# Performance work log

Measured on AMD Instinct MI355X. Metric: run time of the kernel, lower is better.

The kernel has to match this reference:

```python
import jax, jax.numpy as jnp
import numpy as np

N_EMBD = 1024
N_HEAD = 16
HEAD_SIZE = 64


def setup_inputs() -> dict:
    key = jax.random.key(0)
    ks = jax.random.split(key, 6)
    B, T, C, H, D = 2, 2048, N_EMBD, N_HEAD, HEAD_SIZE
    s = 1.0 / np.sqrt(C)
    x = jax.random.normal(ks[0], (B, T, C), dtype=jnp.float32)
    Wq = jax.random.normal(ks[1], (H, C, D), dtype=jnp.float32) * s
    Wk = jax.random.normal(ks[2], (H, C, D), dtype=jnp.float32) * s
    Wv = jax.random.normal(ks[3], (H, C, D), dtype=jnp.float32) * s
    Wo = jax.random.normal(ks[4], (H * D, C), dtype=jnp.float32) * (1.0 / np.sqrt(H * D))
    bo = jax.random.normal(ks[5], (C,), dtype=jnp.float32) * 0.01
    return {"x": x, "Wq": Wq, "Wk": Wk, "Wv": Wv, "Wo": Wo, "bo": bo}


def reference(x, Wq, Wk, Wv, Wo, bo):
    B, T, C = x.shape
    H, _, D = Wq.shape
    # Per-head projections, batched across heads: [B,H,T,D]
    q = jnp.einsum('btc,hcd->bhtd', x, Wq)
    k = jnp.einsum('btc,hcd->bhtd', x, Wk)
    v = jnp.einsum('btc,hcd->bhtd', x, Wv)
    # NOTE: original scales by sqrt(C) = sqrt(n_embd), not sqrt(head_size)
    scale = 1.0 / jnp.sqrt(jnp.float32(C))
    att = jnp.einsum('bhtd,bhsd->bhts', q, k) * scale  # [B,H,T,T]
    causal = jnp.tril(jnp.ones((T, T), dtype=bool))
    att = jnp.where(causal, att, -jnp.inf)
    att = jax.nn.softmax(att, axis=-1)
    # dropout omitted (eval mode / deterministic reference)
    out = jnp.einsum('bhts,bhsd->bhtd', att, v)  # [B,H,T,D]
    out = out.transpose(0, 2, 1, 3).reshape(B, T, H * D)
    return out @ Wo + bo
```

## Files before the change

### kernel.cpp

```cpp
#include <hip/hip_runtime.h>
#include <hip/hip_bf16.h>


typedef __hip_bfloat16 bf16;
typedef __bf16 v8bf __attribute__((ext_vector_type(8)));
typedef float  v4f  __attribute__((ext_vector_type(4)));
typedef unsigned long long u64;
typedef unsigned int u32;

#define MFMA16(a, b, c) __builtin_amdgcn_mfma_f32_16x16x32_bf16((a), (b), (c), 0, 0, 0)

__device__ __forceinline__ bf16 f2b(float x) { return __float2bfloat16(x); }
__device__ __forceinline__ __bf16 f2braw(float x) {
  bf16 t = __float2bfloat16(x);
  return *reinterpret_cast<__bf16*>(&t);
}
__device__ __forceinline__ unsigned short f2bu(float x) {
  bf16 t = __float2bfloat16(x);
  return *reinterpret_cast<unsigned short*>(&t);
}

__device__ __forceinline__ void load16_lds(const bf16* gptr, const bf16* lptr) {
  __builtin_amdgcn_global_load_lds(
      (const __attribute__((address_space(1))) u32*)gptr,
      (__attribute__((address_space(3))) u32*)lptr, 16, 0, 0);
}

__global__ __launch_bounds__(256) void prep_kernel(
    const float* __restrict__ x,
    const float* __restrict__ Wq, const float* __restrict__ Wk,
    const float* __restrict__ Wv, const float* __restrict__ Wo,
    bf16* __restrict__ xb, bf16* __restrict__ wt, bf16* __restrict__ wot)
{
  __shared__ float Lt[32][33];
  const int bid = blockIdx.x, tid = threadIdx.x;

  if (bid < 2048) {
    size_t i = ((size_t)bid * 256 + tid) * 8;
    float4 f0 = *(const float4*)(x + i);
    float4 f1 = *(const float4*)(x + i + 4);
    v8bf v;
    v[0] = f2braw(f0.x); v[1] = f2braw(f0.y); v[2] = f2braw(f0.z); v[3] = f2braw(f0.w);
    v[4] = f2braw(f1.x); v[5] = f2braw(f1.y); v[6] = f2braw(f1.z); v[7] = f2braw(f1.w);
    *(v8bf*)(xb + i) = v;
    return;
  }
  const int tx = tid & 31, ty = tid >> 5;
  if (bid < 5120) {
    const int idx = bid - 2048;
    const int z = idx >> 6, rem = idx & 63;
    const int p = z >> 4, h = z & 15;
    const float* ib = ((p == 0) ? Wq : (p == 1) ? Wk : Wv) + (size_t)h * 65536;
    bf16* ob = wt + (size_t)z * 65536;
    const int j0 = (rem & 1) * 32, i0 = (rem >> 1) * 32;
    #pragma unroll
    for (int r = 0; r < 4; ++r)
      Lt[ty + 8 * r][tx] = ib[(size_t)(i0 + ty + 8 * r) * 64 + j0 + tx];
    __syncthreads();
    #pragma unroll
    for (int r = 0; r < 4; ++r)
      ob[(size_t)(j0 + ty + 8 * r) * 1024 + i0 + tx] = f2b(Lt[tx][ty + 8 * r]);
  } else {
    const int idx = bid - 5120;
    const int j0 = (idx & 31) * 32, i0 = (idx >> 5) * 32;
    #pragma unroll
    for (int r = 0; r < 4; ++r)
      Lt[ty + 8 * r][tx] = Wo[(size_t)(i0 + ty + 8 * r) * 1024 + j0 + tx];
    __syncthreads();
    #pragma unroll
    for (int r = 0; r < 4; ++r)
      wot[(size_t)(j0 + ty + 8 * r) * 1024 + i0 + tx] = f2b(Lt[tx][ty + 8 * r]);
  }
}

__global__ __launch_bounds__(512, 2) void qkv_gemm_kernel(
    const bf16* __restrict__ xb, const bf16* __restrict__ wt,
    bf16* __restrict__ qkv)
{
  __shared__ __align__(16) bf16 Ash[3][256][32];
  __shared__ __align__(16) bf16 Bsh[3][256][32];

  const int mt = blockIdx.x, nt = blockIdx.y;
  const int tid = threadIdx.x, wid = tid >> 6, lane = tid & 63;
  const int ln = lane & 15, quad = lane >> 4;
  const int wm = wid >> 1, wn = wid & 1;
  const int m0 = mt * 256, n0 = nt * 192;

  const v4f vzero = {0.f, 0.f, 0.f, 0.f};
  v4f acc[4][6];
  #pragma unroll
  for (int mf = 0; mf < 4; ++mf)
    #pragma unroll
    for (int nf = 0; nf < 6; ++nf) acc[mf][nf] = vzero;

  const int srow = lane >> 2;
  const int sseg = ((lane & 3) ^ ((lane >> 3) & 3)) * 8;
  const int arow = wid * 32 + srow;
  const int br0 = wid * 32 + srow,  brow0 = (br0 < 192) ? br0 : 191;
  const int br1 = wid * 32 + 16 + srow, brow1 = (br1 < 192) ? br1 : 191;
  const bf16* ga  = xb + (size_t)(m0 + arow) * 1024 + sseg;
  const bf16* gb0 = wt + (size_t)(n0 + brow0) * 1024 + sseg;
  const bf16* gb1 = wt + (size_t)(n0 + brow1) * 1024 + sseg;

  const int fseg = (quad ^ ((ln >> 1) & 3)) * 8;

  #define QSTAGE(BUF) {                                          \
    load16_lds(ga,              &Ash[BUF][wid * 32][0]);         \
    load16_lds(ga + 16 * 1024,  &Ash[BUF][wid * 32 + 16][0]);    \
    load16_lds(gb0,             &Bsh[BUF][wid * 32][0]);         \
    load16_lds(gb1,             &Bsh[BUF][wid * 32 + 16][0]);    \
    ga += 32; gb0 += 32; gb1 += 32; }

  QSTAGE(0)
  QSTAGE(1)

  #define QSTEP(BUF, VM, DOSTAGE)                                          \
  {                                                                        \
    asm volatile("s_waitcnt vmcnt(" #VM ") lgkmcnt(0)" ::: "memory");      \
    __builtin_amdgcn_s_barrier();                                          \
    __builtin_amdgcn_sched_barrier(0);                                     \
    v8bf af[4], bfv[6];                                                    \
    _Pragma("unroll")                                                      \
    for (int mf = 0; mf < 4; ++mf)                                         \
      af[mf] = *(const v8bf*)&Ash[BUF][wm * 64 + mf * 16 + ln][fseg];      \
    _Pragma("unroll")                                                      \
    for (int nf = 0; nf < 6; ++nf)                                         \
      bfv[nf] = *(const v8bf*)&Bsh[BUF][wn * 96 + nf * 16 + ln][fseg];     \
    if (DOSTAGE) QSTAGE((BUF + 2) % 3)                                     \
    __builtin_amdgcn_s_setprio(1);                                         \
    _Pragma("unroll")                                                      \
    for (int mf = 0; mf < 4; ++mf)                                         \
      _Pragma("unroll")                                                    \
      for (int nf = 0; nf < 6; ++nf)                                       \
        acc[mf][nf] = MFMA16(af[mf], bfv[nf], acc[mf][nf]);                \
    __builtin_amdgcn_s_setprio(0);                                         \
  }

  #pragma unroll 1
  for (int it = 0; it < 10; ++it) {
    QSTEP(0, 4, 1)
    QSTEP(1, 4, 1)
    QSTEP(2, 4, 1)
  }
  QSTEP(0, 4, 0)
  QSTEP(1, 0, 0)
  #undef QSTEP
  #undef QSTAGE

  #pragma unroll
  for (int nf = 0; nf < 6; ++nf) {
    const int j = n0 + wn * 96 + nf * 16 + ln;
    const int p = j >> 10;
    const int h = (j >> 6) & 15;
    const int d = j & 63;
    if (p < 2) {
      const float scale = (p == 0) ? 0.0450841149f : 1.0f;
      bf16* base = qkv + (size_t)p * 4194304 + (size_t)h * 262144;
      #pragma unroll
      for (int mf = 0; mf < 4; ++mf)
        #pragma unroll
        for (int r = 0; r < 4; ++r) {
          int m = m0 + wm * 64 + mf * 16 + quad * 4 + r;
          base[(size_t)m * 64 + d] = f2b(acc[mf][nf][r] * scale);
        }
    } else {
      bf16* vb = qkv + (size_t)2 * 4194304 + (size_t)h * 262144;
      #pragma unroll
      for (int mf = 0; mf < 4; ++mf) {
        int mrow = m0 + wm * 64 + mf * 16 + quad * 4;
        int bi = mrow >> 11, t0 = mrow & 2047;
        u64 pk = (u64)f2bu(acc[mf][nf][0]) |
                 ((u64)f2bu(acc[mf][nf][1]) << 16) |
                 ((u64)f2bu(acc[mf][nf][2]) << 32) |
                 ((u64)f2bu(acc[mf][nf][3]) << 48);
        *(u64*)(vb + (size_t)bi * 131072 + (size_t)d * 2048 + t0) = pk;
      }
    }
  }
}

__global__ __launch_bounds__(256, 4) void attn_kernel(
    const bf16* __restrict__ qkv, bf16* __restrict__ att)
{
  union ShU {
    struct { bf16 K[2][64][64]; bf16 V[2][64][64]; } t;
    struct { float O[2][64][36]; float L[2][36]; } c;
  };
  __shared__ __align__(16) ShU sh;

  const int fid = blockIdx.x;
  const int j = fid >> 5;
  const int jr = j & 7, jq = j >> 3;
  const int mt = (jq == 0) ? (31 - jr) : (jq == 1) ? (8 + jr)
               : (jq == 2) ? (23 - jr) : jr;
  const int grp = fid & 31;
  const int b = grp >> 4, h = grp & 15;

  const int tid = threadIdx.x, w = tid >> 6, lane = tid & 63;
  const int ln = lane & 15, quad = lane >> 4;
  const int qh = w & 1, kh = w >> 1;

  const bf16* qbase  = qkv + (size_t)h * 262144 + (size_t)b * 131072;
  const bf16* kbase  = qbase + 4194304;
  const bf16* vtbase = qbase + 8388608;

  const int l8 = lane & 7, r8 = lane >> 3;
  const int slot = l8 ^ r8;
  const int p0 = w * 16 + r8, p1 = p0 + 8;
  const int kp0 = (p0 & 32) | ((p0 & 12) << 1) | ((p0 & 16) >> 2) | (p0 & 3);
  const int kp1 = (p1 & 32) | ((p1 & 12) << 1) | ((p1 & 16) >> 2) | (p1 & 3);
  const bf16* gkp0 = kbase + kp0 * 64 + slot * 8;
  const bf16* gkp1 = kbase + kp1 * 64 + slot * 8;
  const bf16* gvp0 = vtbase + p0 * 2048 + slot * 8;
  const bf16* gvp1 = gvp0 + 8 * 2048;

  const int sw = ln & 7;
  const int cc0 = ((quad    ) ^ sw) * 8;
  const int cc1 = ((quad + 4) ^ sw) * 8;
  const int cck = kh ? cc1 : cc0;
  const int krow0 = (kh * 32 + ln) * 64;
  const int ka0 = krow0 + cc0, ka1 = krow0 + cc1;
  const int voff = ln * 64 + cck;

  v8bf vone;
  {
    unsigned short u = 0x3F80;
    __bf16 e = *reinterpret_cast<__bf16*>(&u);
    #pragma unroll
    for (int jj = 0; jj < 8; ++jj) vone[jj] = e;
  }
  const v4f vzero = {0.f, 0.f, 0.f, 0.f};
  const float NEG = -30000.0f;

  #define STAGE2(BUF) {                                          \
    load16_lds(gkp0, &sh.t.K[BUF][w * 16][0]);                   \
    load16_lds(gkp1, &sh.t.K[BUF][w * 16 + 8][0]);               \
    load16_lds(gvp0, &sh.t.V[BUF][w * 16][0]);                   \
    load16_lds(gvp1, &sh.t.V[BUF][w * 16 + 8][0]);               \
    gkp0 += 4096; gkp1 += 4096; gvp0 += 64; gvp1 += 64; }

  const int row0 = mt * 64;
  const int qrow = row0 + qh * 32;

  v8bf aq[2][2];
  #pragma unroll
  for (int mc = 0; mc < 2; ++mc)
    #pragma unroll
    for (int ks = 0; ks < 2; ++ks)
      aq[mc][ks] = *(const v8bf*)(qbase +
          (size_t)(qrow + mc * 16 + ln) * 64 + ks * 32 + quad * 8);

  v4f o[2][4], lacc[2];
  #pragma unroll
  for (int mc = 0; mc < 2; ++mc) {
    lacc[mc] = vzero;
    #pragma unroll
    for (int dt = 0; dt < 4; ++dt) o[mc][dt] = vzero;
  }

  const int kb_end = mt;
  int kb = 0;
  STAGE2(0)

  #define TILE(BUF)                                                        \
  {                                                                        \
    __syncthreads();                                    \
    const bf16* krB = &sh.t.K[BUF][0][0];                                  \
    const bf16* vrB = &sh.t.V[BUF][0][0];                                  \
    v8bf kf[2][2], vf[4];                                                  \
    kf[0][0] = *(const v8bf*)(krB + ka0);                                  \
    kf[1][0] = *(const v8bf*)(krB + ka1);                                  \
    kf[0][1] = *(const v8bf*)(krB + ka0 + 1024);                           \
    kf[1][1] = *(const v8bf*)(krB + ka1 + 1024);                           \
    vf[0] = *(const v8bf*)(vrB + voff);                                    \
    vf[1] = *(const v8bf*)(vrB + voff + 1024);                             \
    vf[2] = *(const v8bf*)(vrB + voff + 2048);                             \
    vf[3] = *(const v8bf*)(vrB + voff + 3072);                             \
    if (kb < kb_end) STAGE2(BUF ^ 1)                                       \
    _Pragma("unroll")                                                      \
    for (int mc = 0; mc < 2; ++mc) {                                       \
      __builtin_amdgcn_s_setprio(1);                                       \
      v4f s[2];                                                            \
      s[0] = vzero; s[1] = vzero;                                          \
      _Pragma("unroll")                                                    \
      for (int ks = 0; ks < 2; ++ks) {                                     \
        s[0] = MFMA16(kf[ks][0], aq[mc][ks], s[0]);                        \
        s[1] = MFMA16(kf[ks][1], aq[mc][ks], s[1]);                        \
      }                                                                    \
      __builtin_amdgcn_s_setprio(0);                                       \
      const int qg = qrow + mc * 16 + ln;                                  \
      if (kb == kb_end) {                      \
        _Pragma("unroll")                                                  \
        for (int nfl = 0; nfl < 2; ++nfl) {                                \
          const int kc = kb * 64 + kh * 32 + quad * 8 + nfl * 4;           \
          _Pragma("unroll")                                                \
          for (int r = 0; r < 4; ++r)                                      \
            if (kc + r > qg) s[nfl][r] = NEG;                              \
        }                                                                  \
      }                                                                    \
      float ex[2][4];                                                      \
      _Pragma("unroll")                                                    \
      for (int nfl = 0; nfl < 2; ++nfl)                                    \
        _Pragma("unroll")                                                  \
        for (int r = 0; r < 4; ++r)                                        \
          ex[nfl][r] = exp2f(s[nfl][r]);                                   \
      union { u32 uw[4]; v8bf v; } pu;                                     \
      _Pragma("unroll")                                                    \
      for (int nfl = 0; nfl < 2; ++nfl)                                    \
        _Pragma("unroll")                                                  \
        for (int wi = 0; wi < 2; ++wi)                                     \
          asm("v_cvt_pk_bf16_f32 %0, %1, %2"                               \
              : "=v"(pu.uw[nfl * 2 + wi])                                  \
              : "v"(ex[nfl][2 * wi]), "v"(ex[nfl][2 * wi + 1]));           \
      __builtin_amdgcn_s_setprio(1);                                       \
      lacc[mc] = MFMA16(pu.v, vone, lacc[mc]);                             \
      _Pragma("unroll")                                                    \
      for (int dt = 0; dt < 4; ++dt)                                       \
        o[mc][dt] = MFMA16(pu.v, vf[dt], o[mc][dt]);                       \
      __builtin_amdgcn_s_setprio(0);                                       \
    }                                                                      \
  }

  while (true) {
    TILE(0)
    if (kb >= kb_end) break;
    ++kb;
    TILE(1)
    if (kb >= kb_end) break;
    ++kb;
  }
  #undef TILE
  #undef STAGE2

  __syncthreads();
  if (kh == 1) {
    #pragma unroll
    for (int mc = 0; mc < 2; ++mc) {
      #pragma unroll
      for (int dt = 0; dt < 4; ++dt)
        *(v4f*)&sh.c.O[qh][dt * 16 + ln][mc * 16 + quad * 4] = o[mc][dt];
      if (ln == 0)
        *(v4f*)&sh.c.L[qh][mc * 16 + quad * 4] = lacc[mc];
    }
  }
  __syncthreads();
  if (kh == 0) {
    #pragma unroll
    for (int mc = 0; mc < 2; ++mc) {
      v4f pl = *(const v4f*)&sh.c.L[qh][mc * 16 + quad * 4];
      v4f inv;
      #pragma unroll
      for (int r = 0; r < 4; ++r) inv[r] = 1.0f / (lacc[mc][r] + pl[r]);
      #pragma unroll
      for (int dt = 0; dt < 4; ++dt) {
        v4f po = *(const v4f*)&sh.c.O[qh][dt * 16 + ln][mc * 16 + quad * 4];
        #pragma unroll
        for (int r = 0; r < 4; ++r) {
          int m = b * 2048 + qrow + mc * 16 + quad * 4 + r;
          att[(size_t)m * 1024 + h * 64 + dt * 16 + ln] =
              f2b((o[mc][dt][r] + po[r]) * inv[r]);
        }
      }
    }
  }
}

__global__ __launch_bounds__(256) void out_gemm_kernel(
    const bf16* __restrict__ att, const bf16* __restrict__ wot,
    const float* __restrict__ bo, float* __restrict__ out)
{
  __shared__ __align__(16) bf16 Ash[2][128][32];
  __shared__ __align__(16) bf16 Bsh[2][64][32];

  const int mt = blockIdx.x, nt = blockIdx.y;
  const int tid = threadIdx.x, w = tid >> 6, lane = tid & 63;
  const int ln = lane & 15, quad = lane >> 4;
  const int wm = w >> 1, wn = w & 1;
  const int m0 = mt * 128, n0 = nt * 64;

  const v4f vzero = {0.f, 0.f, 0.f, 0.f};
  v4f acc[4][2];
  #pragma unroll
  for (int mf = 0; mf < 4; ++mf)
    #pragma unroll
    for (int nf = 0; nf < 2; ++nf) acc[mf][nf] = vzero;

  const int srow = lane >> 2;
  const int sseg = ((lane & 3) ^ ((lane >> 3) & 3)) * 8;
  const bf16* ga = att + (size_t)(m0 + 32 * w + srow) * 1024 + sseg;
  const bf16* gb = wot + (size_t)(n0 + 16 * w + srow) * 1024 + sseg;

  const int fseg = (quad ^ ((ln >> 1) & 3)) * 8;

  load16_lds(ga,             &Ash[0][32 * w][0]);
  load16_lds(ga + 16 * 1024, &Ash[0][32 * w + 16][0]);
  load16_lds(gb,             &Bsh[0][16 * w][0]);
  ga += 32; gb += 32;

  int kt = 0;
  #define OTILE(BUF)                                                     \
  {                                                                      \
    __syncthreads();                                                     \
    v8bf af[4], bfv[2];                                                  \
    _Pragma("unroll")                                                    \
    for (int mf = 0; mf < 4; ++mf)                                       \
      af[mf] = *(const v8bf*)&Ash[BUF][wm * 64 + mf * 16 + ln][fseg];    \
    _Pragma("unroll")                                                    \
    for (int nf = 0; nf < 2; ++nf)                                       \
      bfv[nf] = *(const v8bf*)&Bsh[BUF][wn * 32 + nf * 16 + ln][fseg];   \
    if (kt < 31) {                                                       \
      load16_lds(ga,             &Ash[BUF ^ 1][32 * w][0]);              \
      load16_lds(ga + 16 * 1024, &Ash[BUF ^ 1][32 * w + 16][0]);         \
      load16_lds(gb,             &Bsh[BUF ^ 1][16 * w][0]);              \
      ga += 32; gb += 32;                                                \
    }                                                                    \
    _Pragma("unroll")                                                    \
    for (int mf = 0; mf < 4; ++mf)                                       \
      _Pragma("unroll")                                                  \
      for (int nf = 0; nf < 2; ++nf)                                     \
        acc[mf][nf] = MFMA16(af[mf], bfv[nf], acc[mf][nf]);              \
    ++kt;                                                                \
  }

  #pragma unroll 1
  for (int it = 0; it < 16; ++it) {
    OTILE(0)
    OTILE(1)
  }
  #undef OTILE

  #pragma unroll
  for (int nf = 0; nf < 2; ++nf) {
    int j = n0 + wn * 32 + nf * 16 + ln;
    float bias = bo[j];
    #pragma unroll
    for (int mf = 0; mf < 4; ++mf)
      #pragma unroll
      for (int r = 0; r < 4; ++r) {
        int m = m0 + wm * 64 + mf * 16 + quad * 4 + r;
        out[(size_t)m * 1024 + j] = acc[mf][nf][r] + bias;
      }
  }
}

extern "C" void kernel_launch(void* const* d_in, const int* in_sizes, int n_in,
                              void* d_out, int out_size, void* d_ws, size_t ws_size,
                              hipStream_t stream) {
  const float* x  = (const float*)d_in[0];
  const float* Wq = (const float*)d_in[1];
  const float* Wk = (const float*)d_in[2];
  const float* Wv = (const float*)d_in[3];
  const float* Wo = (const float*)d_in[4];
  const float* bo = (const float*)d_in[5];
  float* out = (float*)d_out;

  bf16* xb  = (bf16*)d_ws;
  bf16* wt  = xb + 4194304;
  bf16* wot = xb + 7340032;
  bf16* qkv = xb + 8388608;
  bf16* att = xb + 20971520;

  prep_kernel<<<6144, 256, 0, stream>>>(x, Wq, Wk, Wv, Wo, xb, wt, wot);
  qkv_gemm_kernel<<<dim3(16, 16), 512, 0, stream>>>(xb, wt, qkv);
  attn_kernel<<<1024, 256, 0, stream>>>(qkv, att);
  out_gemm_kernel<<<dim3(32, 16), 256, 0, stream>>>(att, wot, bo, out);
}
```

Measured before the change: 165.5 us.

## Load V fragments directly from global and triple-buffer output GEMM pipeline

The attention kernel stops staging V tiles through LDS and instead loads each lane's V fragments straight from global memory (transposed V layout), halving the LDS footprint and the async copies per tile. The output projection GEMM moves from double to triple buffering with explicit vmcnt waits and raw barriers, so two stages of loads stay in flight, and it raises wave priority around the MFMA block. The risk is that direct global V loads are exposed to memory latency inside the tile loop without LDS prefetch. The hand-written waitcnt counts must also match the issued loads exactly.

```diff
diff --git a/kernel.cpp b/kernel.cpp
--- a/kernel.cpp
+++ b/kernel.cpp
@@ -183,7 +183,7 @@
     const bf16* __restrict__ qkv, bf16* __restrict__ att)
 {
   union ShU {
-    struct { bf16 K[2][64][64]; bf16 V[2][64][64]; } t;
+    struct { bf16 K[2][64][64]; } t;
     struct { float O[2][64][36]; float L[2][36]; } c;
   };
   __shared__ __align__(16) ShU sh;
@@ -211,16 +211,13 @@
   const int kp1 = (p1 & 32) | ((p1 & 12) << 1) | ((p1 & 16) >> 2) | (p1 & 3);
   const bf16* gkp0 = kbase + kp0 * 64 + slot * 8;
   const bf16* gkp1 = kbase + kp1 * 64 + slot * 8;
-  const bf16* gvp0 = vtbase + p0 * 2048 + slot * 8;
-  const bf16* gvp1 = gvp0 + 8 * 2048;
 
   const int sw = ln & 7;
   const int cc0 = ((quad    ) ^ sw) * 8;
   const int cc1 = ((quad + 4) ^ sw) * 8;
-  const int cck = kh ? cc1 : cc0;
   const int krow0 = (kh * 32 + ln) * 64;
   const int ka0 = krow0 + cc0, ka1 = krow0 + cc1;
-  const int voff = ln * 64 + cck;
+  const bf16* gvf = vtbase + (size_t)ln * 2048 + kh * 32 + quad * 8;
 
   v8bf vone;
   {
@@ -235,9 +232,7 @@
   #define STAGE2(BUF) {                                          \
     load16_lds(gkp0, &sh.t.K[BUF][w * 16][0]);                   \
     load16_lds(gkp1, &sh.t.K[BUF][w * 16 + 8][0]);               \
-    load16_lds(gvp0, &sh.t.V[BUF][w * 16][0]);                   \
-    load16_lds(gvp1, &sh.t.V[BUF][w * 16 + 8][0]);               \
-    gkp0 += 4096; gkp1 += 4096; gvp0 += 64; gvp1 += 64; }
+    gkp0 += 4096; gkp1 += 4096; }
 
   const int row0 = mt * 64;
   const int qrow = row0 + qh * 32;
@@ -266,16 +261,16 @@
   {                                                                        \
     __syncthreads();                                    \
     const bf16* krB = &sh.t.K[BUF][0][0];                                  \
-    const bf16* vrB = &sh.t.V[BUF][0][0];                                  \
     v8bf kf[2][2], vf[4];                                                  \
     kf[0][0] = *(const v8bf*)(krB + ka0);                                  \
     kf[1][0] = *(const v8bf*)(krB + ka1);                                  \
     kf[0][1] = *(const v8bf*)(krB + ka0 + 1024);                           \
     kf[1][1] = *(const v8bf*)(krB + ka1 + 1024);                           \
-    vf[0] = *(const v8bf*)(vrB + voff);                                    \
-    vf[1] = *(const v8bf*)(vrB + voff + 1024);                             \
-    vf[2] = *(const v8bf*)(vrB + voff + 2048);                             \
-    vf[3] = *(const v8bf*)(vrB + voff + 3072);                             \
+    vf[0] = *(const v8bf*)(gvf);                                           \
+    vf[1] = *(const v8bf*)(gvf + 32768);                                   \
+    vf[2] = *(const v8bf*)(gvf + 65536);                                   \
+    vf[3] = *(const v8bf*)(gvf + 98304);                                   \
+    gvf += 64;                                                             \
     if (kb < kb_end) STAGE2(BUF ^ 1)                                       \
     _Pragma("unroll")                                                      \
     for (int mc = 0; mc < 2; ++mc) {                                       \
@@ -369,8 +364,8 @@
     const bf16* __restrict__ att, const bf16* __restrict__ wot,
     const float* __restrict__ bo, float* __restrict__ out)
 {
-  __shared__ __align__(16) bf16 Ash[2][128][32];
-  __shared__ __align__(16) bf16 Bsh[2][64][32];
+  __shared__ __align__(16) bf16 Ash[3][128][32];
+  __shared__ __align__(16) bf16 Bsh[3][64][32];
 
   const int mt = blockIdx.x, nt = blockIdx.y;
   const int tid = threadIdx.x, w = tid >> 6, lane = tid & 63;
@@ -392,42 +387,47 @@
 
   const int fseg = (quad ^ ((ln >> 1) & 3)) * 8;
 
-  load16_lds(ga,             &Ash[0][32 * w][0]);
-  load16_lds(ga + 16 * 1024, &Ash[0][32 * w + 16][0]);
-  load16_lds(gb,             &Bsh[0][16 * w][0]);
-  ga += 32; gb += 32;
-
-  int kt = 0;
-  #define OTILE(BUF)                                                     \
-  {                                                                      \
-    __syncthreads();                                                     \
-    v8bf af[4], bfv[2];                                                  \
-    _Pragma("unroll")                                                    \
-    for (int mf = 0; mf < 4; ++mf)                                       \
-      af[mf] = *(const v8bf*)&Ash[BUF][wm * 64 + mf * 16 + ln][fseg];    \
-    _Pragma("unroll")                                                    \
-    for (int nf = 0; nf < 2; ++nf)                                       \
-      bfv[nf] = *(const v8bf*)&Bsh[BUF][wn * 32 + nf * 16 + ln][fseg];   \
-    if (kt < 31) {                                                       \
-      load16_lds(ga,             &Ash[BUF ^ 1][32 * w][0]);              \
-      load16_lds(ga + 16 * 1024, &Ash[BUF ^ 1][32 * w + 16][0]);         \
-      load16_lds(gb,             &Bsh[BUF ^ 1][16 * w][0]);              \
-      ga += 32; gb += 32;                                                \
-    }                                                                    \
-    _Pragma("unroll")                                                    \
-    for (int mf = 0; mf < 4; ++mf)                                       \
-      _Pragma("unroll")                                                  \
-      for (int nf = 0; nf < 2; ++nf)                                     \
-        acc[mf][nf] = MFMA16(af[mf], bfv[nf], acc[mf][nf]);              \
-    ++kt;                                                                \
+  #define OSTAGE(BUF) {                                          \
+    load16_lds(ga,             &Ash[BUF][32 * w][0]);            \
+    load16_lds(ga + 16 * 1024, &Ash[BUF][32 * w + 16][0]);       \
+    load16_lds(gb,             &Bsh[BUF][16 * w][0]);            \
+    ga += 32; gb += 32; }
+
+  OSTAGE(0)
+  OSTAGE(1)
+
+  #define OSTEP(BUF, VM, DOSTAGE)                                          \
+  {                                                                        \
+    asm volatile("s_waitcnt vmcnt(" #VM ") lgkmcnt(0)" ::: "memory");      \
+    __builtin_amdgcn_s_barrier();                                          \
+    __builtin_amdgcn_sched_barrier(0);                                     \
+    v8bf af[4], bfv[2];                                                    \
+    _Pragma("unroll")                                                      \
+    for (int mf = 0; mf < 4; ++mf)                                         \
+      af[mf] = *(const v8bf*)&Ash[BUF][wm * 64 + mf * 16 + ln][fseg];      \
+    _Pragma("unroll")                                                      \
+    for (int nf = 0; nf < 2; ++nf)                                         \
+      bfv[nf] = *(const v8bf*)&Bsh[BUF][wn * 32 + nf * 16 + ln][fseg];     \
+    if (DOSTAGE) OSTAGE((BUF + 2) % 3)                                     \
+    __builtin_amdgcn_s_setprio(1);                                         \
+    _Pragma("unroll")                                                      \
+    for (int mf = 0; mf < 4; ++mf)                                         \
+      _Pragma("unroll")                                                    \
+      for (int nf = 0; nf < 2; ++nf)                                       \
+        acc[mf][nf] = MFMA16(af[mf], bfv[nf], acc[mf][nf]);                \
+    __builtin_amdgcn_s_setprio(0);                                         \
   }
 
   #pragma unroll 1
-  for (int it = 0; it < 16; ++it) {
-    OTILE(0)
-    OTILE(1)
-  }
-  #undef OTILE
+  for (int it = 0; it < 10; ++it) {
+    OSTEP(0, 3, 1)
+    OSTEP(1, 3, 1)
+    OSTEP(2, 3, 1)
+  }
+  OSTEP(0, 3, 0)
+  OSTEP(1, 0, 0)
+  #undef OSTEP
+  #undef OSTAGE
 
   #pragma unroll
   for (int nf = 0; nf < 2; ++nf) {
```

Result: slower. 175.0 us (+5.7%).
